# Optimization experiments

Measured on AMD Instinct MI355X. Metric: run time of the kernel, lower is better.

Reference implementation:

```python
import jax, jax.numpy as jnp
import numpy as np


def setup_inputs() -> dict:
    key = jax.random.key(0)
    ks = jax.random.split(key, 8)
    N, E = 100000, 3200000
    IN, H, OUT = 256, 128, 64
    x = jax.random.normal(ks[0], (N, IN), dtype=jnp.float32)
    src = jax.random.randint(ks[1], (E,), 0, N, dtype=jnp.int64)
    dst = jax.random.randint(ks[2], (E,), 0, N, dtype=jnp.int64)
    # Glorot-ish scaled weights
    W1_self = jax.random.normal(ks[3], (IN, H), dtype=jnp.float32) / np.sqrt(IN)
    W1_neigh = jax.random.normal(ks[4], (IN, H), dtype=jnp.float32) / np.sqrt(IN)
    b1 = jnp.zeros((H,), dtype=jnp.float32)
    W2_self = jax.random.normal(ks[5], (H, OUT), dtype=jnp.float32) / np.sqrt(H)
    W2_neigh = jax.random.normal(ks[6], (H, OUT), dtype=jnp.float32) / np.sqrt(H)
    b2 = jnp.zeros((OUT,), dtype=jnp.float32)
    return {"x": x, "src": src, "dst": dst,
            "W1_self": W1_self, "W1_neigh": W1_neigh, "b1": b1,
            "W2_self": W2_self, "W2_neigh": W2_neigh, "b2": b2}


def _sage_mean(h, src, dst, W_self, W_neigh, b, deg_inv):
    # mean aggregation over in-neighbors (edges src -> dst)
    N = h.shape[0]
    agg = jax.ops.segment_sum(h[src], dst, num_segments=N)  # [N, F]
    h_neigh = agg * deg_inv[:, None]
    return h @ W_self + h_neigh @ W_neigh + b


def reference(x, src, dst, W1_self, W1_neigh, b1, W2_self, W2_neigh, b2):
    N = x.shape[0]
    deg = jax.ops.segment_sum(jnp.ones_like(dst, dtype=x.dtype), dst, num_segments=N)
    deg_inv = 1.0 / jnp.maximum(deg, 1.0)  # DGL clamps in-degree to >= 1
    h = _sage_mean(x, src, dst, W1_self, W1_neigh, b1, deg_inv)
    h = jax.nn.relu(h)
    h = _sage_mean(h, src, dst, W2_self, W2_neigh, b2, deg_inv)
    return h
```

## Files before the change

### kernel.cpp

```cpp
#include <hip/hip_runtime.h>
#include <hip/hip_bf16.h>


typedef unsigned int uint32;
typedef __attribute__((ext_vector_type(8))) short short8;
typedef __attribute__((ext_vector_type(4))) float f32x4;
typedef __attribute__((ext_vector_type(2))) float f32x2;

#define NBMAX 1024
#define NQMAX 32
#define EPB   4096

#if defined(__has_builtin)
#if __has_builtin(__builtin_amdgcn_cvt_pk_f32_fp8) && __has_builtin(__builtin_amdgcn_cvt_pk_fp8_f32)
#define FP8_HW 1
#endif
#endif
#ifndef FP8_HW
#define FP8_HW 0
#endif

__device__ __forceinline__ unsigned short f2bf(float f) {
    unsigned u = __float_as_uint(f);
    u += 0x7fffu + ((u >> 16) & 1u);
    return (unsigned short)(u >> 16);
}
__device__ __forceinline__ uint32 pack2bf(float lo, float hi) {
    return (uint32)f2bf(lo) | ((uint32)f2bf(hi) << 16);
}
__device__ __forceinline__ float bf_lo(uint32 v) { return __uint_as_float(v << 16); }
__device__ __forceinline__ float bf_hi(uint32 v) { return __uint_as_float(v & 0xFFFF0000u); }

__device__ __forceinline__ unsigned char enc8(float v) {
#if FP8_HW
    return (unsigned char)(__builtin_amdgcn_cvt_pk_fp8_f32(v, v, 0, false) & 0xFF);
#else
    float g = v * 0x1p-120f;
    uint32 b = __float_as_uint(g);
    uint32 s = (b >> 24) & 0x80u;
    b &= 0x7fffffffu;
    b += 0x7ffffu + ((b >> 20) & 1u);
    int t = (int)(b >> 20) - 960;
    t = t < 0 ? 0 : (t > 126 ? 126 : t);
    return (unsigned char)(s | (uint32)t);
#endif
}
#if !FP8_HW
__device__ __forceinline__ float dec1(uint32 b) {
    uint32 bits = ((b & 0x80u) << 24) | ((b & 0x7fu) << 20);
    return __uint_as_float(bits) * 0x1p+120f;
}
#endif

template<bool HI>
__device__ __forceinline__ f32x2 cvt2(uint32 u) {
#if FP8_HW
    auto t = __builtin_amdgcn_cvt_pk_f32_fp8(u, HI);
    f32x2 r; r[0] = t[0]; r[1] = t[1];
    return r;
#else
    uint32 a = HI ? (u >> 16) : u;
    f32x2 r; r[0] = dec1(a & 0xffu); r[1] = dec1((a >> 8) & 0xffu);
    return r;
#endif
}

__device__ __forceinline__ void acc8(f32x2* acc, uint2 v) {
    acc[0] += cvt2<false>(v.x); acc[1] += cvt2<true>(v.x);
    acc[2] += cvt2<false>(v.y); acc[3] += cvt2<true>(v.y);
}

__device__ __forceinline__ f32x2 shfl_xor2(f32x2 v, int m) {
    union { f32x2 f; long long l; } u;
    u.f = v;
    u.l = __shfl_xor(u.l, m);
    return u.f;
}

__global__ __launch_bounds__(256) void k_hist_fine(const int* __restrict__ dst, int E,
                                                   int* __restrict__ bcnt) {
    __shared__ int hist[NBMAX];
    for (int i = threadIdx.x; i < NBMAX; i += 256) hist[i] = 0;
    __syncthreads();
    int base = blockIdx.x * EPB;
    #pragma unroll 4
    for (int i = 0; i < EPB / 256; ++i) {
        int e = base + i * 256 + threadIdx.x;
        if (e < E) atomicAdd(&hist[dst[e] >> 7], 1);
    }
    __syncthreads();
    for (int i = threadIdx.x; i < NBMAX; i += 256) {
        int h = hist[i];
        if (h) atomicAdd(&bcnt[i], h);
    }
}

__global__ __launch_bounds__(1024) void k_scan(const int* __restrict__ bcnt, int NBF, int NQ,
                                               int* __restrict__ boffs, int* __restrict__ gfill_fine,
                                               int* __restrict__ gfillq, int E) {
    __shared__ int sd[1024];
    int tid = threadIdx.x;
    int v = (tid < NBF) ? bcnt[tid] : 0;
    sd[tid] = v;
    __syncthreads();
    for (int off = 1; off < 1024; off <<= 1) {
        int t = (tid >= off) ? sd[tid - off] : 0;
        __syncthreads();
        sd[tid] += t;
        __syncthreads();
    }
    int excl = sd[tid] - v;
    if (tid < NBF) { boffs[tid] = excl; gfill_fine[tid] = excl; }
    if (tid == 0) boffs[NBF] = E;
    __syncthreads();
    if (tid < NQ) {
        int f = tid * 32;
        gfillq[tid] = (f < NBF) ? (sd[f] - ((f < NBF) ? bcnt[f] : 0)) : E;
    }
}

__global__ __launch_bounds__(256) void k_scatter_coarse(const int* __restrict__ src,
                                                        const int* __restrict__ dst, int E,
                                                        int* __restrict__ gfillq,
                                                        uint32* __restrict__ pairs1) {
    __shared__ int hist[NQMAX];
    __shared__ int basea[NQMAX];
    if (threadIdx.x < NQMAX) hist[threadIdx.x] = 0;
    __syncthreads();
    int base = blockIdx.x * EPB;
    #pragma unroll 4
    for (int i = 0; i < EPB / 256; ++i) {
        int e = base + i * 256 + threadIdx.x;
        if (e < E) atomicAdd(&hist[dst[e] >> 12], 1);
    }
    __syncthreads();
    if (threadIdx.x < NQMAX) {
        int h = hist[threadIdx.x];
        basea[threadIdx.x] = h ? atomicAdd(&gfillq[threadIdx.x], h) : 0;
        hist[threadIdx.x] = 0;
    }
    __syncthreads();
    #pragma unroll 4
    for (int i = 0; i < EPB / 256; ++i) {
        int e = base + i * 256 + threadIdx.x;
        if (e < E) {
            int d = dst[e];
            int q = d >> 12;
            int pos = basea[q] + atomicAdd(&hist[q], 1);
            pairs1[pos] = ((uint32)src[e] << 12) | (uint32)(d & 4095);
        }
    }
}

__global__ __launch_bounds__(256) void k_scatter_fine(const uint32* __restrict__ pairs1,
                                                      const int* __restrict__ boffs,
                                                      const int* __restrict__ qend,
                                                      int* __restrict__ gfill_fine,
                                                      uint32* __restrict__ pairs2, int NC) {
    __shared__ int hist[32];
    __shared__ int basea[32];
    const int q = blockIdx.x;
    const int s0 = boffs[q * 32];
    const int s1 = qend[q];
    for (long cb = (long)s0 + (long)blockIdx.y * EPB; cb < s1; cb += (long)NC * EPB) {
        int cend = (int)((cb + EPB < s1) ? cb + EPB : s1);
        if (threadIdx.x < 32) hist[threadIdx.x] = 0;
        __syncthreads();
        for (int e = (int)cb + threadIdx.x; e < cend; e += 256)
            atomicAdd(&hist[(pairs1[e] >> 7) & 31], 1);
        __syncthreads();
        if (threadIdx.x < 32) {
            int h = hist[threadIdx.x];
            basea[threadIdx.x] = h ? atomicAdd(&gfill_fine[q * 32 + threadIdx.x], h) : 0;
            hist[threadIdx.x] = 0;
        }
        __syncthreads();
        for (int e = (int)cb + threadIdx.x; e < cend; e += 256) {
            uint32 p = pairs1[e];
            int fl = (p >> 7) & 31;
            int pos = basea[fl] + atomicAdd(&hist[fl], 1);
            pairs2[pos] = p;
        }
        __syncthreads();
    }
}

__global__ __launch_bounds__(256) void k_bucket_sort(const uint32* __restrict__ pairs,
                                                     const int* __restrict__ boffs,
                                                     int N, int E,
                                                     int* __restrict__ row_start,
                                                     float* __restrict__ deg_inv,
                                                     int* __restrict__ src_sorted) {
    __shared__ int cnt[128];
    __shared__ int sc[128];
    __shared__ int fill[128];
    int b = blockIdx.x, tid = threadIdx.x;
    int s0 = boffs[b], s1 = boffs[b + 1];
    if (tid < 128) cnt[tid] = 0;
    __syncthreads();
    for (int e = s0 + tid; e < s1; e += 256)
        atomicAdd(&cnt[pairs[e] & 127], 1);
    __syncthreads();
    if (tid < 128) sc[tid] = cnt[tid];
    __syncthreads();
    for (int off = 1; off < 128; off <<= 1) {
        int v = 0;
        if (tid < 128 && tid >= off) v = sc[tid - off];
        __syncthreads();
        if (tid < 128) sc[tid] += v;
        __syncthreads();
    }
    if (tid < 128) {
        int excl = sc[tid] - cnt[tid];
        int node = b * 128 + tid;
        if (node < N) {
            row_start[node] = s0 + excl;
            int d = cnt[tid];
            deg_inv[node] = 1.0f / (float)(d > 1 ? d : 1);
        }
        fill[tid] = s0 + excl;
    }
    if (b == 0 && tid == 0) row_start[N] = E;
    __syncthreads();
    for (int e = s0 + tid; e < s1; e += 256) {
        uint32 p = pairs[e];
        int pos = atomicAdd(&fill[p & 127], 1);
        src_sorted[pos] = (int)(p >> 12);
    }
}

__global__ __launch_bounds__(256) void k_cast_x(const float* __restrict__ x, uint32* __restrict__ xb,
                                                long n8, long total8) {
    long t = (long)blockIdx.x * blockDim.x + threadIdx.x;
    if (t >= total8) return;
    uint4 o = make_uint4(0u, 0u, 0u, 0u);
    if (t < n8) {
        const float4* p = reinterpret_cast<const float4*>(x) + t * 2;
        float4 a = p[0], b = p[1];
        o.x = pack2bf(a.x, a.y); o.y = pack2bf(a.z, a.w);
        o.z = pack2bf(b.x, b.y); o.w = pack2bf(b.z, b.w);
    }
    reinterpret_cast<uint4*>(xb)[t] = o;
}

__global__ __launch_bounds__(256) void k_wt(const float* __restrict__ Ws, const float* __restrict__ Wn,
                                            int K, int logK, int halfC, unsigned short* __restrict__ Wt) {
    int t = blockIdx.x * blockDim.x + threadIdx.x;
    int total = 2 * halfC * K;
    if (t >= total) return;
    int c = t >> logK, k = t & (K - 1);
    float v = (c < halfC) ? Ws[(size_t)k * halfC + c] : Wn[(size_t)k * halfC + (c - halfC)];
    Wt[t] = f2bf(v);
}

template<int K, int NF, bool YSPLIT>
__global__ __launch_bounds__(512) void gemm_rs(const unsigned short* __restrict__ A, int nstrip,
                                               const unsigned short* __restrict__ Wt,
                                               unsigned short* __restrict__ S16,
                                               unsigned char* __restrict__ N8) {
    constexpr int KS = K / 32;
    __shared__ unsigned short Bs[NF * KS * 512];
    const int tid = threadIdx.x;
    const int wave = tid >> 6, lane = tid & 63;
    const int l15 = lane & 15, l4 = lane >> 4;

    const unsigned short* Wtblk = Wt + (YSPLIT ? (size_t)blockIdx.y * 128 * K : 0);
    const bool out8 = YSPLIT && (blockIdx.y == 1);

    for (int i = tid; i < NF * KS * 64; i += 512) {
        int f = i >> 6, l = i & 63;
        int s = f / NF, n = f - s * NF;
        int col = n * 16 + (l & 15);
        int k = s * 32 + (l >> 4) * 8;
        uint4 v = *reinterpret_cast<const uint4*>(&Wtblk[(size_t)col * K + k]);
        *reinterpret_cast<uint4*>(&Bs[(size_t)i * 8]) = v;
    }
    __syncthreads();

    const unsigned short* Bl = Bs + (size_t)lane * 8;
    const int stride = gridDim.x;
    int g = blockIdx.x;
    if (g >= nstrip) return;

    uint4 uA[KS], uB[KS];

    auto loadA = [&](int gg, uint4* u) {
        int arow = gg * 128 + wave * 16 + l15;
        const unsigned short* Ar = A + (size_t)arow * K + l4 * 8;
        #pragma unroll
        for (int s = 0; s < KS; ++s)
            u[s] = *reinterpret_cast<const uint4*>(Ar + s * 32);
    };

    auto compute = [&](int gc, uint4* u) {
        f32x4 acc[NF] = {};
        #pragma unroll
        for (int s = 0; s < KS; ++s) {
            union { uint4 q; short8 v; } cv;
            cv.q = u[s];
            short8 af = cv.v;
            #pragma unroll
            for (int n = 0; n < NF; ++n) {
                short8 bf = *reinterpret_cast<const short8*>(Bl + (size_t)(s * NF + n) * 512);
                acc[n] = __builtin_amdgcn_mfma_f32_16x16x32_bf16(af, bf, acc[n], 0, 0, 0);
            }
        }
        const int rbase = gc * 128 + wave * 16;
        #pragma unroll
        for (int n = 0; n < NF; ++n) {
            #pragma unroll
            for (int r = 0; r < 4; ++r) {
                int rw = rbase + l4 * 4 + r;
                if constexpr (YSPLIT) {
                    int col = n * 16 + l15;
                    if (out8) N8[(size_t)rw * 128 + col] = enc8(acc[n][r]);
                    else      S16[(size_t)rw * 128 + col] = f2bf(acc[n][r]);
                } else {
                    if (n < 4) S16[(size_t)rw * 64 + n * 16 + l15] = f2bf(acc[n][r]);
                    else       N8[(size_t)rw * 64 + (n - 4) * 16 + l15] = enc8(acc[n][r]);
                }
            }
        }
    };

    loadA(g, uA);
    while (true) {
        int gn = g + stride;
        if (gn < nstrip) loadA(gn, uB);
        compute(g, uA);
        if (gn >= nstrip) break;
        g = gn;
        gn = g + stride;
        if (gn < nstrip) loadA(gn, uA);
        compute(g, uB);
        if (gn >= nstrip) break;
        g = gn;
    }
}

__global__ __launch_bounds__(256) void k_agg1(const uint2* __restrict__ t1n, const uint4* __restrict__ t1s,
                                              const int* __restrict__ rs, const int* __restrict__ ss,
                                              const float* __restrict__ dinv, const float* __restrict__ b1,
                                              uint4* __restrict__ h, int N) {
    int wid  = (blockIdx.x * blockDim.x + threadIdx.x) >> 6;
    int lane = threadIdx.x & 63;
    if (wid >= N) return;
    int e0 = rs[wid], e1 = rs[wid + 1];
    const int q = lane >> 4, c = lane & 15;
    f32x2 acc[4] = {};
    int e = e0;
    for (; e + 16 <= e1; e += 16) {
        int s0 = ss[e + q];
        int s1 = ss[e + 4 + q];
        int s2 = ss[e + 8 + q];
        int s3 = ss[e + 12 + q];
        uint2 v0 = t1n[(size_t)s0 * 16 + c];
        uint2 v1 = t1n[(size_t)s1 * 16 + c];
        uint2 v2 = t1n[(size_t)s2 * 16 + c];
        uint2 v3 = t1n[(size_t)s3 * 16 + c];
        acc8(acc, v0); acc8(acc, v1); acc8(acc, v2); acc8(acc, v3);
    }
    for (; e < e1; e += 4) {
        if (e + q < e1) {
            uint2 v = t1n[(size_t)ss[e + q] * 16 + c];
            acc8(acc, v);
        }
    }
    #pragma unroll
    for (int j = 0; j < 4; ++j) {
        acc[j] += shfl_xor2(acc[j], 16);
        acc[j] += shfl_xor2(acc[j], 32);
    }
    if (lane < 16) {
        float di = dinv[wid];
        uint4 sv = t1s[(size_t)wid * 16 + c];
        float4 bA = *reinterpret_cast<const float4*>(&b1[c * 8]);
        float4 bB = *reinterpret_cast<const float4*>(&b1[c * 8 + 4]);
        float h0 = fmaxf(fmaf(acc[0][0], di, bf_lo(sv.x)) + bA.x, 0.f);
        float h1 = fmaxf(fmaf(acc[0][1], di, bf_hi(sv.x)) + bA.y, 0.f);
        float h2 = fmaxf(fmaf(acc[1][0], di, bf_lo(sv.y)) + bA.z, 0.f);
        float h3 = fmaxf(fmaf(acc[1][1], di, bf_hi(sv.y)) + bA.w, 0.f);
        float h4 = fmaxf(fmaf(acc[2][0], di, bf_lo(sv.z)) + bB.x, 0.f);
        float h5 = fmaxf(fmaf(acc[2][1], di, bf_hi(sv.z)) + bB.y, 0.f);
        float h6 = fmaxf(fmaf(acc[3][0], di, bf_lo(sv.w)) + bB.z, 0.f);
        float h7 = fmaxf(fmaf(acc[3][1], di, bf_hi(sv.w)) + bB.w, 0.f);
        uint4 o;
        o.x = pack2bf(h0, h1); o.y = pack2bf(h2, h3);
        o.z = pack2bf(h4, h5); o.w = pack2bf(h6, h7);
        h[(size_t)wid * 16 + c] = o;
    }
}

__global__ __launch_bounds__(256) void k_agg2(const uint2* __restrict__ t2n, const uint4* __restrict__ t2s,
                                              const int* __restrict__ rs, const int* __restrict__ ss,
                                              const float* __restrict__ dinv, const float* __restrict__ b2,
                                              float* __restrict__ out, int N) {
    int wid  = (blockIdx.x * blockDim.x + threadIdx.x) >> 6;
    int lane = threadIdx.x & 63;
    if (wid >= N) return;
    int e0 = rs[wid], e1 = rs[wid + 1];
    const int q = lane >> 3, c = lane & 7;
    f32x2 acc[4] = {};
    int e = e0;
    for (; e + 32 <= e1; e += 32) {
        int s0 = ss[e + q];
        int s1 = ss[e + 8 + q];
        int s2 = ss[e + 16 + q];
        int s3 = ss[e + 24 + q];
        uint2 v0 = t2n[(size_t)s0 * 8 + c];
        uint2 v1 = t2n[(size_t)s1 * 8 + c];
        uint2 v2 = t2n[(size_t)s2 * 8 + c];
        uint2 v3 = t2n[(size_t)s3 * 8 + c];
        acc8(acc, v0); acc8(acc, v1); acc8(acc, v2); acc8(acc, v3);
    }
    for (; e < e1; e += 8) {
        if (e + q < e1) {
            uint2 v = t2n[(size_t)ss[e + q] * 8 + c];
            acc8(acc, v);
        }
    }
    #pragma unroll
    for (int j = 0; j < 4; ++j) {
        acc[j] += shfl_xor2(acc[j], 8);
        acc[j] += shfl_xor2(acc[j], 16);
        acc[j] += shfl_xor2(acc[j], 32);
    }
    if (lane < 8) {
        float di = dinv[wid];
        uint4 sv = t2s[(size_t)wid * 8 + c];
        float4 bA = *reinterpret_cast<const float4*>(&b2[c * 8]);
        float4 bB = *reinterpret_cast<const float4*>(&b2[c * 8 + 4]);
        float4 oA, oB;
        oA.x = fmaf(acc[0][0], di, bf_lo(sv.x)) + bA.x;
        oA.y = fmaf(acc[0][1], di, bf_hi(sv.x)) + bA.y;
        oA.z = fmaf(acc[1][0], di, bf_lo(sv.y)) + bA.z;
        oA.w = fmaf(acc[1][1], di, bf_hi(sv.y)) + bA.w;
        oB.x = fmaf(acc[2][0], di, bf_lo(sv.z)) + bB.x;
        oB.y = fmaf(acc[2][1], di, bf_hi(sv.z)) + bB.y;
        oB.z = fmaf(acc[3][0], di, bf_lo(sv.w)) + bB.z;
        oB.w = fmaf(acc[3][1], di, bf_hi(sv.w)) + bB.w;
        *reinterpret_cast<float4*>(&out[(size_t)wid * 64 + c * 8]) = oA;
        *reinterpret_cast<float4*>(&out[(size_t)wid * 64 + c * 8 + 4]) = oB;
    }
}

extern "C" void kernel_launch(void* const* d_in, const int* in_sizes, int n_in,
                              void* d_out, int out_size, void* d_ws, size_t ws_size,
                              hipStream_t stream) {
    const float* x   = (const float*)d_in[0];
    const int*   src = (const int*)d_in[1];
    const int*   dst = (const int*)d_in[2];
    const float* W1s = (const float*)d_in[3];
    const float* W1n = (const float*)d_in[4];
    const float* b1  = (const float*)d_in[5];
    const float* W2s = (const float*)d_in[6];
    const float* W2n = (const float*)d_in[7];
    const float* b2  = (const float*)d_in[8];
    float* out = (float*)d_out;

    const int IN = 256, H = 128, OUT = 64;
    const int N  = in_sizes[0] / IN;
    const int E  = in_sizes[1];
    const int Mpad = (N + 127) & ~127;
    const int NBF = (N + 127) >> 7;
    const int NQ  = (N + 4095) >> 12;

    char* ws = (char*)d_ws;
    size_t off = 0;
    auto alloc = [&](size_t bytes) -> char* {
        char* p = ws + off;
        off = (off + bytes + 255) & ~(size_t)255;
        return p;
    };
    int*   row_start  = (int*)  alloc((size_t)(N + 1) * 4);
    float* deg_inv    = (float*)alloc((size_t)N * 4);
    int*   bcnt       = (int*)  alloc((size_t)NBMAX * 4);
    int*   boffs      = (int*)  alloc((size_t)(NBMAX + 1) * 4);
    int*   gfill_fine = (int*)  alloc((size_t)NBMAX * 4);
    int*   gfillq     = (int*)  alloc((size_t)NQMAX * 4);
    int*   src_sorted = (int*)  alloc((size_t)E * 4);
    uint32* pairs1    = (uint32*)alloc((size_t)E * 4);
    uint32* pairs2    = (uint32*)alloc((size_t)E * 4);
    unsigned short* xb  = (unsigned short*)alloc((size_t)Mpad * IN * 2);
    unsigned short* Wt1 = (unsigned short*)alloc((size_t)(2 * H) * IN * 2);
    unsigned short* Wt2 = (unsigned short*)alloc((size_t)(2 * OUT) * H * 2);
    unsigned short* t1s = (unsigned short*)alloc((size_t)Mpad * H * 2);
    unsigned char*  t1n = (unsigned char*) alloc((size_t)Mpad * H);
    unsigned short* hbf = (unsigned short*)alloc((size_t)Mpad * H * 2);

    hipMemsetAsync(bcnt, 0, (size_t)NBMAX * 4, stream);
    int nblk = (E + EPB - 1) / EPB;
    k_hist_fine     <<<nblk, 256, 0, stream>>>(dst, E, bcnt);
    k_scan          <<<1, 1024, 0, stream>>>(bcnt, NBF, NQ, boffs, gfill_fine, gfillq, E);
    k_scatter_coarse<<<nblk, 256, 0, stream>>>(src, dst, E, gfillq, pairs1);
    k_scatter_fine  <<<dim3(NQ, 32), 256, 0, stream>>>(pairs1, boffs, gfillq, gfill_fine, pairs2, 32);
    k_bucket_sort   <<<NBF, 256, 0, stream>>>(pairs2, boffs, N, E, row_start, deg_inv, src_sorted);

    long n8 = (long)N * IN / 8, total8 = (long)Mpad * IN / 8;
    k_cast_x<<<(int)((total8 + 255) / 256), 256, 0, stream>>>(x, (uint32*)xb, n8, total8);
    k_wt<<<(2 * H * IN + 255) / 256, 256, 0, stream>>>(W1s, W1n, IN, 8, H, Wt1);
    k_wt<<<(2 * OUT * H + 255) / 256, 256, 0, stream>>>(W2s, W2n, H, 7, OUT, Wt2);

    int nstrip1 = Mpad / 128;
    gemm_rs<256, 8, true><<<dim3(256, 2), 512, 0, stream>>>(xb, nstrip1, Wt1, t1s, t1n);
    k_agg1<<<(N + 3) / 4, 256, 0, stream>>>((const uint2*)t1n, (const uint4*)t1s,
                                            row_start, src_sorted, deg_inv, b1, (uint4*)hbf, N);
    int nstrip2 = Mpad / 128;
    gemm_rs<128, 8, false><<<dim3(256, 1), 512, 0, stream>>>(hbf, nstrip2, Wt2, t1s, t1n);
    k_agg2<<<(N + 3) / 4, 256, 0, stream>>>((const uint2*)t1n, (const uint4*)t1s,
                                            row_start, src_sorted, deg_inv, b2, out, N);
}
```

Before: 304.1 us.

## Fuse layer-2 GEMM into layer-1 aggregation kernel via per-block MFMA

The layer-1 aggregation kernel now processes 16 nodes per block and keeps the resulting ReLU'd hidden rows in shared memory. It then multiplies them by the layer-2 weights with bf16 MFMA and writes t2s (bf16) and t2n (fp8) directly. This removes the hbf round trip through global memory and the separate layer-2 GEMM launch. In exchange, each block reloads the full 32 KB Wt2 into LDS, and the larger shared-memory footprint may reduce occupancy for the latency-bound gather.

```diff
diff --git a/kernel.cpp b/kernel.cpp
--- a/kernel.cpp
+++ b/kernel.cpp
@@ -338,56 +338,110 @@
     }
 }
 
-__global__ __launch_bounds__(256) void k_agg1(const uint2* __restrict__ t1n, const uint4* __restrict__ t1s,
-                                              const int* __restrict__ rs, const int* __restrict__ ss,
-                                              const float* __restrict__ dinv, const float* __restrict__ b1,
-                                              uint4* __restrict__ h, int N) {
-    int wid  = (blockIdx.x * blockDim.x + threadIdx.x) >> 6;
-    int lane = threadIdx.x & 63;
-    if (wid >= N) return;
-    int e0 = rs[wid], e1 = rs[wid + 1];
+__global__ __launch_bounds__(256) void k_agg1f(const uint2* __restrict__ t1n, const uint4* __restrict__ t1s,
+                                               const int* __restrict__ rs, const int* __restrict__ ss,
+                                               const float* __restrict__ dinv, const float* __restrict__ b1,
+                                               const unsigned short* __restrict__ Wt2,
+                                               unsigned short* __restrict__ t2s,
+                                               unsigned char* __restrict__ t2n, int N) {
+    __shared__ unsigned short Bs[32 * 512];
+    __shared__ unsigned short Hs[16 * 136];
+    const int tid = threadIdx.x;
+    const int wave = tid >> 6, lane = tid & 63;
+    const int l15 = lane & 15, l4 = lane >> 4;
+
+    for (int i = tid; i < 32 * 64; i += 256) {
+        int f = i >> 6, l = i & 63;
+        int s = f >> 3, n = f & 7;
+        int col = n * 16 + (l & 15);
+        int k = s * 32 + (l >> 4) * 8;
+        uint4 v = *reinterpret_cast<const uint4*>(&Wt2[(size_t)col * 128 + k]);
+        *reinterpret_cast<uint4*>(&Bs[(size_t)i * 8]) = v;
+    }
+
+    const int nb = blockIdx.x * 16;
     const int q = lane >> 4, c = lane & 15;
-    f32x2 acc[4] = {};
-    int e = e0;
-    for (; e + 16 <= e1; e += 16) {
-        int s0 = ss[e + q];
-        int s1 = ss[e + 4 + q];
-        int s2 = ss[e + 8 + q];
-        int s3 = ss[e + 12 + q];
-        uint2 v0 = t1n[(size_t)s0 * 16 + c];
-        uint2 v1 = t1n[(size_t)s1 * 16 + c];
-        uint2 v2 = t1n[(size_t)s2 * 16 + c];
-        uint2 v3 = t1n[(size_t)s3 * 16 + c];
-        acc8(acc, v0); acc8(acc, v1); acc8(acc, v2); acc8(acc, v3);
-    }
-    for (; e < e1; e += 4) {
-        if (e + q < e1) {
-            uint2 v = t1n[(size_t)ss[e + q] * 16 + c];
-            acc8(acc, v);
-        }
-    }
+
+    for (int j = 0; j < 4; ++j) {
+        int wid = nb + wave * 4 + j;
+        int row = wave * 4 + j;
+        if (wid < N) {
+            int e0 = rs[wid], e1 = rs[wid + 1];
+            f32x2 acc[4] = {};
+            int e = e0;
+            for (; e + 16 <= e1; e += 16) {
+                int s0 = ss[e + q];
+                int s1 = ss[e + 4 + q];
+                int s2 = ss[e + 8 + q];
+                int s3 = ss[e + 12 + q];
+                uint2 v0 = t1n[(size_t)s0 * 16 + c];
+                uint2 v1 = t1n[(size_t)s1 * 16 + c];
+                uint2 v2 = t1n[(size_t)s2 * 16 + c];
+                uint2 v3 = t1n[(size_t)s3 * 16 + c];
+                acc8(acc, v0); acc8(acc, v1); acc8(acc, v2); acc8(acc, v3);
+            }
+            for (; e < e1; e += 4) {
+                if (e + q < e1) {
+                    uint2 v = t1n[(size_t)ss[e + q] * 16 + c];
+                    acc8(acc, v);
+                }
+            }
+            #pragma unroll
+            for (int t = 0; t < 4; ++t) {
+                acc[t] += shfl_xor2(acc[t], 16);
+                acc[t] += shfl_xor2(acc[t], 32);
+            }
+            if (lane < 16) {
+                float di = dinv[wid];
+                uint4 sv = t1s[(size_t)wid * 16 + c];
+                float4 bA = *reinterpret_cast<const float4*>(&b1[c * 8]);
+                float4 bB = *reinterpret_cast<const float4*>(&b1[c * 8 + 4]);
+                float h0 = fmaxf(fmaf(acc[0][0], di, bf_lo(sv.x)) + bA.x, 0.f);
+                float h1 = fmaxf(fmaf(acc[0][1], di, bf_hi(sv.x)) + bA.y, 0.f);
+                float h2 = fmaxf(fmaf(acc[1][0], di, bf_lo(sv.y)) + bA.z, 0.f);
+                float h3 = fmaxf(fmaf(acc[1][1], di, bf_hi(sv.y)) + bA.w, 0.f);
+                float h4 = fmaxf(fmaf(acc[2][0], di, bf_lo(sv.z)) + bB.x, 0.f);
+                float h5 = fmaxf(fmaf(acc[2][1], di, bf_hi(sv.z)) + bB.y, 0.f);
+                float h6 = fmaxf(fmaf(acc[3][0], di, bf_lo(sv.w)) + bB.z, 0.f);
+                float h7 = fmaxf(fmaf(acc[3][1], di, bf_hi(sv.w)) + bB.w, 0.f);
+                uint4 o;
+                o.x = pack2bf(h0, h1); o.y = pack2bf(h2, h3);
+                o.z = pack2bf(h4, h5); o.w = pack2bf(h6, h7);
+                *reinterpret_cast<uint4*>(&Hs[row * 136 + lane * 8]) = o;
+            }
+        } else if (lane < 16) {
+            uint4 z = make_uint4(0u, 0u, 0u, 0u);
+            *reinterpret_cast<uint4*>(&Hs[row * 136 + lane * 8]) = z;
+        }
+    }
+    __syncthreads();
+
+    const unsigned short* Bl = Bs + (size_t)lane * 8;
+    f32x4 acc2[2] = {};
     #pragma unroll
-    for (int j = 0; j < 4; ++j) {
-        acc[j] += shfl_xor2(acc[j], 16);
-        acc[j] += shfl_xor2(acc[j], 32);
-    }
-    if (lane < 16) {
-        float di = dinv[wid];
-        uint4 sv = t1s[(size_t)wid * 16 + c];
-        float4 bA = *reinterpret_cast<const float4*>(&b1[c * 8]);
-        float4 bB = *reinterpret_cast<const float4*>(&b1[c * 8 + 4]);
-        float h0 = fmaxf(fmaf(acc[0][0], di, bf_lo(sv.x)) + bA.x, 0.f);
-        float h1 = fmaxf(fmaf(acc[0][1], di, bf_hi(sv.x)) + bA.y, 0.f);
-        float h2 = fmaxf(fmaf(acc[1][0], di, bf_lo(sv.y)) + bA.z, 0.f);
-        float h3 = fmaxf(fmaf(acc[1][1], di, bf_hi(sv.y)) + bA.w, 0.f);
-        float h4 = fmaxf(fmaf(acc[2][0], di, bf_lo(sv.z)) + bB.x, 0.f);
-        float h5 = fmaxf(fmaf(acc[2][1], di, bf_hi(sv.z)) + bB.y, 0.f);
-        float h6 = fmaxf(fmaf(acc[3][0], di, bf_lo(sv.w)) + bB.z, 0.f);
-        float h7 = fmaxf(fmaf(acc[3][1], di, bf_hi(sv.w)) + bB.w, 0.f);
-        uint4 o;
-        o.x = pack2bf(h0, h1); o.y = pack2bf(h2, h3);
-        o.z = pack2bf(h4, h5); o.w = pack2bf(h6, h7);
-        h[(size_t)wid * 16 + c] = o;
+    for (int s = 0; s < 4; ++s) {
+        union { uint4 qq; short8 v; } cv;
+        cv.qq = *reinterpret_cast<const uint4*>(&Hs[l15 * 136 + s * 32 + l4 * 8]);
+        short8 af = cv.v;
+        #pragma unroll
+        for (int t = 0; t < 2; ++t) {
+            int n = wave * 2 + t;
+            short8 bf = *reinterpret_cast<const short8*>(Bl + (size_t)(s * 8 + n) * 512);
+            acc2[t] = __builtin_amdgcn_mfma_f32_16x16x32_bf16(af, bf, acc2[t], 0, 0, 0);
+        }
+    }
+    #pragma unroll
+    for (int t = 0; t < 2; ++t) {
+        int n = wave * 2 + t;
+        #pragma unroll
+        for (int r = 0; r < 4; ++r) {
+            int rw = nb + l4 * 4 + r;
+            if (rw < N) {
+                int col = n * 16 + l15;
+                if (n < 4) t2s[(size_t)rw * 64 + col] = f2bf(acc2[t][r]);
+                else       t2n[(size_t)rw * 64 + (col - 64)] = enc8(acc2[t][r]);
+            }
+        }
     }
 }
 
@@ -486,7 +540,8 @@
     unsigned short* Wt2 = (unsigned short*)alloc((size_t)(2 * OUT) * H * 2);
     unsigned short* t1s = (unsigned short*)alloc((size_t)Mpad * H * 2);
     unsigned char*  t1n = (unsigned char*) alloc((size_t)Mpad * H);
-    unsigned short* hbf = (unsigned short*)alloc((size_t)Mpad * H * 2);
+    unsigned short* t2s = (unsigned short*)alloc((size_t)Mpad * OUT * 2);
+    unsigned char*  t2n = (unsigned char*) alloc((size_t)Mpad * OUT);
 
     hipMemsetAsync(bcnt, 0, (size_t)NBMAX * 4, stream);
     int nblk = (E + EPB - 1) / EPB;
@@ -503,10 +558,9 @@
 
     int nstrip1 = Mpad / 128;
     gemm_rs<256, 8, true><<<dim3(256, 2), 512, 0, stream>>>(xb, nstrip1, Wt1, t1s, t1n);
-    k_agg1<<<(N + 3) / 4, 256, 0, stream>>>((const uint2*)t1n, (const uint4*)t1s,
-                                            row_start, src_sorted, deg_inv, b1, (uint4*)hbf, N);
-    int nstrip2 = Mpad / 128;
-    gemm_rs<128, 8, false><<<dim3(256, 1), 512, 0, stream>>>(hbf, nstrip2, Wt2, t1s, t1n);
-    k_agg2<<<(N + 3) / 4, 256, 0, stream>>>((const uint2*)t1n, (const uint4*)t1s,
+    k_agg1f<<<(N + 15) / 16, 256, 0, stream>>>((const uint2*)t1n, (const uint4*)t1s,
+                                               row_start, src_sorted, deg_inv, b1, Wt2,
+                                               t2s, t2n, N);
+    k_agg2<<<(N + 3) / 4, 256, 0, stream>>>((const uint2*)t2n, (const uint4*)t2s,
                                             row_start, src_sorted, deg_inv, b2, out, N);
 }
```

Measured after the change: 355.9 us. +17.0%, slower.
